# Optimization experiments

Measured on AMD Instinct MI355X. Metric: run time of the kernel, lower is better.

## Reference

```python
import jax, jax.numpy as jnp
import numpy as np

N = 50000       # nodes
E = 1600000     # edges (avg degree 32)
DIM = 256       # args.dim (input feature dim)
OUT = 64        # args.n_classes (output dim)
ALPHA = 0.2     # leaky relu negative slope


def setup_inputs() -> dict:
    key = jax.random.key(0)
    k1, k2, k3, k4 = jax.random.split(key, 4)
    x = jax.random.normal(k1, (N, DIM), dtype=jnp.float32)
    # sparse adjacency as COO indices: row 0 = src (output row), row 1 = dst (neighbor)
    edge_index = jax.random.randint(k2, (2, E), 0, N, dtype=jnp.int32)
    # xavier-uniform init as in SpGraphAttentionLayer
    lim_w = float(np.sqrt(6.0 / (DIM + OUT)))
    W = jax.random.uniform(k3, (DIM, OUT), minval=-lim_w, maxval=lim_w, dtype=jnp.float32)
    lim_a = float(np.sqrt(6.0 / (1 + 2 * OUT)))
    a = jax.random.uniform(k4, (2 * OUT,), minval=-lim_a, maxval=lim_a, dtype=jnp.float32)
    return {"x": x, "edge_index": edge_index, "W": W, "a": a}


def reference(x, edge_index, W, a):
    # h = x @ W : [N, OUT]
    h = x @ W
    src = edge_index[0]  # [E] output row index i
    dst = edge_index[1]  # [E] neighbor index j
    # attention logit per edge: a . concat(h[i], h[j])
    logits = h[src] @ a[:OUT] + h[dst] @ a[OUT:]          # [E]
    # edge_e = exp(-leakyrelu(logits))  (note the negation, as in SpGraphAttentionLayer)
    e = jnp.exp(-jax.nn.leaky_relu(logits, ALPHA))         # [E]
    # row-wise normalizer: sum_j e_ij
    rowsum = jax.ops.segment_sum(e, src, num_segments=N)   # [N]
    # aggregated messages: sum_j e_ij * h_j
    agg = jax.ops.segment_sum(e[:, None] * h[dst], src, num_segments=N)  # [N, OUT]
    # h' = agg / rowsum, then elu (concat=True branch)
    return jax.nn.elu(agg / rowsum[:, None])
```

## Files before the change

kernel.cpp:

```cpp
#include <hip/hip_runtime.h>

#define NN 50000
#define NE 1600000
#define DIM 256
#define OUTD 64
#define ALPHA 0.2f

#define BSH 6
#define NB ((NN + 63) >> 6)
#define CAP 3072
#define P1 250
#define EPB (NE / P1)

#define GB1024 ((NN + 255) / 256)
#define FAT_GRID (GB1024 + P1)
#define WSTRIDE 264

typedef unsigned short u16;
typedef unsigned int u32;
typedef __attribute__((ext_vector_type(8))) short short8;
typedef __attribute__((ext_vector_type(4))) float floatx4;

__device__ __forceinline__ u16 f2bf(float f) {
  u32 b = __float_as_uint(f);
  b += 0x7FFFu + ((b >> 16) & 1u);
  return (u16)(b >> 16);
}
__device__ __forceinline__ float bflo(u32 u) { return __uint_as_float(u << 16); }
__device__ __forceinline__ float bfhi(u32 u) { return __uint_as_float(u & 0xFFFF0000u); }

__global__ __launch_bounds__(256) void init_kernel(const float* __restrict__ W,
                                                   u32* __restrict__ wt,
                                                   int* __restrict__ bktcnt) {
  if (blockIdx.x < 4) {
    const int i = blockIdx.x * 256 + threadIdx.x;
    if (i < NB) bktcnt[i] = 0;
    return;
  }
  const int g = (blockIdx.x - 4) * 256 + threadIdx.x;
  const int n = g >> 7;
  const int kp = g & 127;
  const float lo = W[(size_t)(2 * kp) * OUTD + n];
  const float hi = W[(size_t)(2 * kp + 1) * OUTD + n];
  wt[g] = (u32)f2bf(lo) | ((u32)f2bf(hi) << 16);
}

__global__ __launch_bounds__(1024) void fat_kernel(
    const float* __restrict__ x, const u32* __restrict__ wt,
    const float* __restrict__ a, u16* __restrict__ hb,
    float* __restrict__ s1, float* __restrict__ s2,
    const int* __restrict__ src, const int* __restrict__ dst,
    int* __restrict__ bktcnt, u32* __restrict__ binned)
{
  __shared__ u16 Wl[OUTD * WSTRIDE];
  int* lh = (int*)Wl;
  const int t = threadIdx.x;

  if (blockIdx.x < GB1024) {
    {
      const uint4* srcv = (const uint4*)wt;
#pragma unroll
      for (int i = 0; i < 2; ++i) {
        const int c = t + 1024 * i;
        const int n = c >> 5;
        const int k8 = c & 31;
        *(uint4*)&Wl[n * WSTRIDE + k8 * 8] = srcv[c];
      }
    }
    __syncthreads();

    const int lane = t & 63;
    const int wv = t >> 6;
    const int n = lane & 15;
    const int quad = lane >> 4;
    int rb = blockIdx.x * 256 + wv * 16;
    if (rb > NN - 16) rb = NN - 16;
    const int row = rb + n;
    const float4* xrow = (const float4*)(x + (size_t)row * DIM);

    floatx4 acc[4] = {{0.f, 0.f, 0.f, 0.f},
                      {0.f, 0.f, 0.f, 0.f},
                      {0.f, 0.f, 0.f, 0.f},
                      {0.f, 0.f, 0.f, 0.f}};

#pragma unroll
    for (int kk = 0; kk < 8; ++kk) {
      const float4 lo = xrow[kk * 8 + quad * 2];
      const float4 hi = xrow[kk * 8 + quad * 2 + 1];
      union { u32 u[4]; short8 s; } af;
      af.u[0] = (u32)f2bf(lo.x) | ((u32)f2bf(lo.y) << 16);
      af.u[1] = (u32)f2bf(lo.z) | ((u32)f2bf(lo.w) << 16);
      af.u[2] = (u32)f2bf(hi.x) | ((u32)f2bf(hi.y) << 16);
      af.u[3] = (u32)f2bf(hi.z) | ((u32)f2bf(hi.w) << 16);
#pragma unroll
      for (int nt = 0; nt < 4; ++nt) {
        const short8 bf =
            *(const short8*)&Wl[(nt * 16 + n) * WSTRIDE + kk * 32 + quad * 8];
        acc[nt] = __builtin_amdgcn_mfma_f32_16x16x32_bf16(af.s, bf, acc[nt], 0, 0, 0);
      }
    }

    float av1[4], av2[4];
#pragma unroll
    for (int nt = 0; nt < 4; ++nt) {
      av1[nt] = a[nt * 16 + n];
      av2[nt] = a[OUTD + nt * 16 + n];
    }

#pragma unroll
    for (int reg = 0; reg < 4; ++reg) {
      const int r = rb + quad * 4 + reg;
      float q1 = acc[0][reg] * av1[0] + acc[1][reg] * av1[1] +
                 acc[2][reg] * av1[2] + acc[3][reg] * av1[3];
      float q2 = acc[0][reg] * av2[0] + acc[1][reg] * av2[1] +
                 acc[2][reg] * av2[2] + acc[3][reg] * av2[3];
#pragma unroll
      for (int off = 1; off <= 8; off <<= 1) {
        q1 += __shfl_xor(q1, off);
        q2 += __shfl_xor(q2, off);
      }
      if (n == 0) { s1[r] = q1; s2[r] = q2; }
#pragma unroll
      for (int nt = 0; nt < 4; ++nt)
        hb[(size_t)r * OUTD + nt * 16 + n] = f2bf(acc[nt][reg]);
    }
    return;
  }

  const int p = blockIdx.x - GB1024;
  for (int i = t; i < NB; i += 1024) lh[i] = 0;
  __syncthreads();

  const int4* src4 = (const int4*)(src + p * EPB);
  const int4* dst4 = (const int4*)(dst + p * EPB);
  for (int i = t; i < EPB / 4; i += 1024) {
    const int4 s = src4[i];
    if ((u32)s.x < (u32)NN) atomicAdd(&lh[s.x >> BSH], 1);
    if ((u32)s.y < (u32)NN) atomicAdd(&lh[s.y >> BSH], 1);
    if ((u32)s.z < (u32)NN) atomicAdd(&lh[s.z >> BSH], 1);
    if ((u32)s.w < (u32)NN) atomicAdd(&lh[s.w >> BSH], 1);
  }
  __syncthreads();

  for (int b = t; b < NB; b += 1024) {
    const int c = lh[b];
    lh[b] = (c > 0) ? atomicAdd(bktcnt + b, c) + b * CAP : 0;
  }
  __syncthreads();

  for (int i = t; i < EPB / 4; i += 1024) {
    const int4 s = src4[i];
    const int4 d = dst4[i];
    int pos, b;
    if ((u32)s.x < (u32)NN) {
      b = s.x >> BSH; pos = atomicAdd(&lh[b], 1);
      if (pos < (b + 1) * CAP) binned[pos] = ((u32)(s.x & 63) << 16) | (u32)(d.x & 0xFFFF);
    }
    if ((u32)s.y < (u32)NN) {
      b = s.y >> BSH; pos = atomicAdd(&lh[b], 1);
      if (pos < (b + 1) * CAP) binned[pos] = ((u32)(s.y & 63) << 16) | (u32)(d.y & 0xFFFF);
    }
    if ((u32)s.z < (u32)NN) {
      b = s.z >> BSH; pos = atomicAdd(&lh[b], 1);
      if (pos < (b + 1) * CAP) binned[pos] = ((u32)(s.z & 63) << 16) | (u32)(d.z & 0xFFFF);
    }
    if ((u32)s.w < (u32)NN) {
      b = s.w >> BSH; pos = atomicAdd(&lh[b], 1);
      if (pos < (b + 1) * CAP) binned[pos] = ((u32)(s.w & 63) << 16) | (u32)(d.w & 0xFFFF);
    }
  }
}

__global__ __launch_bounds__(512) void bucket_agg_kernel(
    const u16* __restrict__ hb, const float* __restrict__ s1,
    const float* __restrict__ s2, const int* __restrict__ bktcnt,
    const u32* __restrict__ binned, float* __restrict__ out)
{
  __shared__ u16 sdst[CAP];
  __shared__ float wls[CAP];
  __shared__ float s1l[64];
  __shared__ int cnt[64];
  __shared__ int off0[64];
  __shared__ int cur[64];
  const int b = blockIdx.x;
  const int t = threadIdx.x;
  int n = bktcnt[b];
  if (n > CAP) n = CAP;

  if (t < 64) {
    cnt[t] = 0;
    const int nd = b * 64 + t;
    s1l[t] = (nd < NN) ? s1[nd] : 0.f;
  }
  __syncthreads();

  const u32* eb = binned + (size_t)b * CAP;
  for (int i = t; i < n; i += 512)
    atomicAdd(&cnt[(eb[i] >> 16) & 63], 1);
  __syncthreads();

  if (t < 64) {
    const int v = cnt[t];
    int xx = v;
#pragma unroll
    for (int o = 1; o < 64; o <<= 1) {
      const int y = __shfl_up(xx, o, 64);
      if (t >= o) xx += y;
    }
    off0[t] = xx - v;
    cur[t] = xx - v;
  }
  __syncthreads();

  for (int i = t; i < n; i += 512) {
    const u32 v = eb[i];
    const int ln = (v >> 16) & 63;
    const int d = (int)(v & 0xFFFFu);
    const int pos = atomicAdd(&cur[ln], 1);
    sdst[pos] = (u16)d;
    const float logit = s1l[ln] + s2[d];
    const float lr = logit > 0.f ? logit : ALPHA * logit;
    wls[pos] = __expf(-lr);
  }
  __syncthreads();

  const int lane = t & 63;
  const int wv = t >> 6;
  const int g = lane >> 3;
  const int seg = lane & 7;
  const int ln = wv * 8 + g;
  const int node = b * 64 + ln;
  const int base = off0[ln];
  const int myc = cnt[ln];

  float a0 = 0.f, a1 = 0.f, a2 = 0.f, a3 = 0.f;
  float a4 = 0.f, a5 = 0.f, a6 = 0.f, a7 = 0.f;
  float wsum = 0.f;

  int e = 0;
  for (; e + 3 < myc; e += 4) {
    const int dg0 = sdst[base + e];      const float wg0 = wls[base + e];
    const int dg1 = sdst[base + e + 1];  const float wg1 = wls[base + e + 1];
    const int dg2 = sdst[base + e + 2];  const float wg2 = wls[base + e + 2];
    const int dg3 = sdst[base + e + 3];  const float wg3 = wls[base + e + 3];
    const uint4 p0 = *(const uint4*)(hb + (size_t)dg0 * OUTD + seg * 8);
    const uint4 p1 = *(const uint4*)(hb + (size_t)dg1 * OUTD + seg * 8);
    const uint4 p2 = *(const uint4*)(hb + (size_t)dg2 * OUTD + seg * 8);
    const uint4 p3 = *(const uint4*)(hb + (size_t)dg3 * OUTD + seg * 8);
    a0 = fmaf(wg0, bflo(p0.x), a0); a1 = fmaf(wg0, bfhi(p0.x), a1);
    a2 = fmaf(wg0, bflo(p0.y), a2); a3 = fmaf(wg0, bfhi(p0.y), a3);
    a4 = fmaf(wg0, bflo(p0.z), a4); a5 = fmaf(wg0, bfhi(p0.z), a5);
    a6 = fmaf(wg0, bflo(p0.w), a6); a7 = fmaf(wg0, bfhi(p0.w), a7);
    wsum += wg0;
    a0 = fmaf(wg1, bflo(p1.x), a0); a1 = fmaf(wg1, bfhi(p1.x), a1);
    a2 = fmaf(wg1, bflo(p1.y), a2); a3 = fmaf(wg1, bfhi(p1.y), a3);
    a4 = fmaf(wg1, bflo(p1.z), a4); a5 = fmaf(wg1, bfhi(p1.z), a5);
    a6 = fmaf(wg1, bflo(p1.w), a6); a7 = fmaf(wg1, bfhi(p1.w), a7);
    wsum += wg1;
    a0 = fmaf(wg2, bflo(p2.x), a0); a1 = fmaf(wg2, bfhi(p2.x), a1);
    a2 = fmaf(wg2, bflo(p2.y), a2); a3 = fmaf(wg2, bfhi(p2.y), a3);
    a4 = fmaf(wg2, bflo(p2.z), a4); a5 = fmaf(wg2, bfhi(p2.z), a5);
    a6 = fmaf(wg2, bflo(p2.w), a6); a7 = fmaf(wg2, bfhi(p2.w), a7);
    wsum += wg2;
    a0 = fmaf(wg3, bflo(p3.x), a0); a1 = fmaf(wg3, bfhi(p3.x), a1);
    a2 = fmaf(wg3, bflo(p3.y), a2); a3 = fmaf(wg3, bfhi(p3.y), a3);
    a4 = fmaf(wg3, bflo(p3.z), a4); a5 = fmaf(wg3, bfhi(p3.z), a5);
    a6 = fmaf(wg3, bflo(p3.w), a6); a7 = fmaf(wg3, bfhi(p3.w), a7);
    wsum += wg3;
  }
  for (; e < myc; ++e) {
    const int dg = sdst[base + e];
    const float wg = wls[base + e];
    const uint4 p = *(const uint4*)(hb + (size_t)dg * OUTD + seg * 8);
    a0 = fmaf(wg, bflo(p.x), a0);
    a1 = fmaf(wg, bfhi(p.x), a1);
    a2 = fmaf(wg, bflo(p.y), a2);
    a3 = fmaf(wg, bfhi(p.y), a3);
    a4 = fmaf(wg, bflo(p.z), a4);
    a5 = fmaf(wg, bfhi(p.z), a5);
    a6 = fmaf(wg, bflo(p.w), a6);
    a7 = fmaf(wg, bfhi(p.w), a7);
    wsum += wg;
  }

  if (node < NN) {
    const float inv = (myc > 0) ? 1.f / wsum : 0.f;
    float4 r;
    float v;
    v = a0 * inv; r.x = v > 0.f ? v : (__expf(v) - 1.f);
    v = a1 * inv; r.y = v > 0.f ? v : (__expf(v) - 1.f);
    v = a2 * inv; r.z = v > 0.f ? v : (__expf(v) - 1.f);
    v = a3 * inv; r.w = v > 0.f ? v : (__expf(v) - 1.f);
    *(float4*)(out + (size_t)node * OUTD + seg * 8) = r;
    v = a4 * inv; r.x = v > 0.f ? v : (__expf(v) - 1.f);
    v = a5 * inv; r.y = v > 0.f ? v : (__expf(v) - 1.f);
    v = a6 * inv; r.z = v > 0.f ? v : (__expf(v) - 1.f);
    v = a7 * inv; r.w = v > 0.f ? v : (__expf(v) - 1.f);
    *(float4*)(out + (size_t)node * OUTD + seg * 8 + 4) = r;
  }
}

extern "C" void kernel_launch(void* const* d_in, const int* in_sizes, int n_in,
                              void* d_out, int out_size, void* d_ws, size_t ws_size,
                              hipStream_t stream) {
  const float* x = (const float*)d_in[0];
  const int* ei = (const int*)d_in[1];
  const float* W = (const float*)d_in[2];
  const float* a = (const float*)d_in[3];
  float* out = (float*)d_out;

  u16* hb = (u16*)d_ws;
  float* s1 = (float*)(hb + (size_t)NN * OUTD);
  float* s2 = s1 + NN;
  int* bktcnt = (int*)(s2 + NN);
  u32* wt = (u32*)(bktcnt + NB);
  u32* binned = wt + 8192;

  const int* src = ei;
  const int* dst = ei + NE;

  hipLaunchKernelGGL(init_kernel, dim3(36), dim3(256), 0, stream, W, wt, bktcnt);
  hipLaunchKernelGGL(fat_kernel, dim3(FAT_GRID), dim3(1024), 0, stream,
                     x, wt, a, hb, s1, s2, src, dst, bktcnt, binned);
  hipLaunchKernelGGL(bucket_agg_kernel, dim3(NB), dim3(512), 0, stream,
                     hb, s1, s2, bktcnt, binned, out);
}
```

Before: 141.4 us.

## Stage edges in LDS and counting-sort per block before coalesced binned writes

The binning blocks now load each chunk of edges into shared memory, build a per-block bucket histogram, run a block-wide prefix scan, and scatter the edges into a locally sorted buffer. They then write to global binned storage contiguously, so writes for the same bucket land in consecutive addresses instead of being scattered. This costs a much larger shared-memory allocation, about 56KB, for the fat kernel, which may lower occupancy for the GEMM blocks that share it. It also adds a 10-step scan with barriers and a second pass over the edges in LDS.

```diff
diff --git a/kernel.cpp b/kernel.cpp
--- a/kernel.cpp
+++ b/kernel.cpp
@@ -15,6 +15,7 @@
 #define GB1024 ((NN + 255) / 256)
 #define FAT_GRID (GB1024 + P1)
 #define WSTRIDE 264
+#define SMEMW (2 * EPB + 1024 + 2 * NB)
 
 typedef unsigned short u16;
 typedef unsigned int u32;
@@ -52,8 +53,8 @@
     const int* __restrict__ src, const int* __restrict__ dst,
     int* __restrict__ bktcnt, u32* __restrict__ binned)
 {
-  __shared__ u16 Wl[OUTD * WSTRIDE];
-  int* lh = (int*)Wl;
+  __shared__ u32 smem[SMEMW];
+  u16* Wl = (u16*)smem;
   const int t = threadIdx.x;
 
   if (blockIdx.x < GB1024) {
@@ -128,46 +129,76 @@
   }
 
   const int p = blockIdx.x - GB1024;
-  for (int i = t; i < NB; i += 1024) lh[i] = 0;
-  __syncthreads();
-
-  const int4* src4 = (const int4*)(src + p * EPB);
-  const int4* dst4 = (const int4*)(dst + p * EPB);
-  for (int i = t; i < EPB / 4; i += 1024) {
-    const int4 s = src4[i];
-    if ((u32)s.x < (u32)NN) atomicAdd(&lh[s.x >> BSH], 1);
-    if ((u32)s.y < (u32)NN) atomicAdd(&lh[s.y >> BSH], 1);
-    if ((u32)s.z < (u32)NN) atomicAdd(&lh[s.z >> BSH], 1);
-    if ((u32)s.w < (u32)NN) atomicAdd(&lh[s.w >> BSH], 1);
-  }
-  __syncthreads();
-
-  for (int b = t; b < NB; b += 1024) {
-    const int c = lh[b];
-    lh[b] = (c > 0) ? atomicAdd(bktcnt + b, c) + b * CAP : 0;
-  }
-  __syncthreads();
-
-  for (int i = t; i < EPB / 4; i += 1024) {
-    const int4 s = src4[i];
-    const int4 d = dst4[i];
-    int pos, b;
-    if ((u32)s.x < (u32)NN) {
-      b = s.x >> BSH; pos = atomicAdd(&lh[b], 1);
-      if (pos < (b + 1) * CAP) binned[pos] = ((u32)(s.x & 63) << 16) | (u32)(d.x & 0xFFFF);
-    }
-    if ((u32)s.y < (u32)NN) {
-      b = s.y >> BSH; pos = atomicAdd(&lh[b], 1);
-      if (pos < (b + 1) * CAP) binned[pos] = ((u32)(s.y & 63) << 16) | (u32)(d.y & 0xFFFF);
-    }
-    if ((u32)s.z < (u32)NN) {
-      b = s.z >> BSH; pos = atomicAdd(&lh[b], 1);
-      if (pos < (b + 1) * CAP) binned[pos] = ((u32)(s.z & 63) << 16) | (u32)(d.z & 0xFFFF);
-    }
-    if ((u32)s.w < (u32)NN) {
-      b = s.w >> BSH; pos = atomicAdd(&lh[b], 1);
-      if (pos < (b + 1) * CAP) binned[pos] = ((u32)(s.w & 63) << 16) | (u32)(d.w & 0xFFFF);
-    }
+  u32* ebuf = smem;
+  u32* sorted = smem + EPB;
+  int* scn = (int*)(smem + 2 * EPB);
+  int* gbase = (int*)(smem + 2 * EPB + 1024);
+  int* cur = gbase + NB;
+
+  scn[t] = 0;
+  __syncthreads();
+
+  {
+    const int4* src4 = (const int4*)(src + p * EPB);
+    const int4* dst4 = (const int4*)(dst + p * EPB);
+    for (int i = t; i < EPB / 4; i += 1024) {
+      const int4 s = src4[i];
+      const int4 d = dst4[i];
+      u32 v0 = ((u32)s.x < (u32)NN) ? (((u32)s.x << 16) | ((u32)d.x & 0xFFFFu)) : 0xFFFFFFFFu;
+      u32 v1 = ((u32)s.y < (u32)NN) ? (((u32)s.y << 16) | ((u32)d.y & 0xFFFFu)) : 0xFFFFFFFFu;
+      u32 v2 = ((u32)s.z < (u32)NN) ? (((u32)s.z << 16) | ((u32)d.z & 0xFFFFu)) : 0xFFFFFFFFu;
+      u32 v3 = ((u32)s.w < (u32)NN) ? (((u32)s.w << 16) | ((u32)d.w & 0xFFFFu)) : 0xFFFFFFFFu;
+      ebuf[i * 4 + 0] = v0;
+      ebuf[i * 4 + 1] = v1;
+      ebuf[i * 4 + 2] = v2;
+      ebuf[i * 4 + 3] = v3;
+      if (v0 != 0xFFFFFFFFu) atomicAdd(&scn[v0 >> 22], 1);
+      if (v1 != 0xFFFFFFFFu) atomicAdd(&scn[v1 >> 22], 1);
+      if (v2 != 0xFFFFFFFFu) atomicAdd(&scn[v2 >> 22], 1);
+      if (v3 != 0xFFFFFFFFu) atomicAdd(&scn[v3 >> 22], 1);
+    }
+  }
+  __syncthreads();
+
+  {
+    int xx = scn[t];
+    for (int o = 1; o < 1024; o <<= 1) {
+      const int y = (t >= o) ? scn[t - o] : 0;
+      __syncthreads();
+      xx += y;
+      scn[t] = xx;
+      __syncthreads();
+    }
+  }
+
+  if (t < NB) {
+    const int incl = scn[t];
+    const int excl = (t > 0) ? scn[t - 1] : 0;
+    const int c = incl - excl;
+    cur[t] = excl;
+    if (c > 0) {
+      const int gb = atomicAdd(bktcnt + t, c) + t * CAP;
+      gbase[t] = gb - excl;
+    }
+  }
+  __syncthreads();
+
+  for (int i = t; i < EPB; i += 1024) {
+    const u32 v = ebuf[i];
+    if (v != 0xFFFFFFFFu) {
+      const int pos = atomicAdd(&cur[v >> 22], 1);
+      sorted[pos] = v;
+    }
+  }
+  __syncthreads();
+
+  const int total = scn[NB - 1];
+  for (int i = t; i < total; i += 1024) {
+    const u32 v = sorted[i];
+    const int b = v >> 22;
+    const int pos = gbase[b] + i;
+    if (pos < (b + 1) * CAP)
+      binned[pos] = (((v >> 16) & 63u) << 16) | (v & 0xFFFFu);
   }
 }
 
```

After: 139.1 us, median of 3. About the same (-1.6%).
